# Optimization experiments

Measured on AMD Instinct MI355X. Metric: run time of the kernel, lower is better.

## Reference

```python
import jax, jax.numpy as jnp
import numpy as np

NEG_SLOPE = 0.2  # PyG GATConv default negative_slope


def _gat_layer(x, src, dst, n_nodes, W, a_src, a_dst, b):
    # x: [N, din]; src/dst: [E] (self-loops already included)
    h = x @ W                                  # [N, dout]
    s_src = h @ a_src                          # [N]
    s_dst = h @ a_dst                          # [N]
    e = jax.nn.leaky_relu(s_src[src] + s_dst[dst], NEG_SLOPE)  # [E]
    # per-target-node softmax over incoming edges (stable via segment max)
    m = jax.ops.segment_max(e, dst, num_segments=n_nodes)      # [N]
    a = jnp.exp(e - m[dst])                    # [E]
    denom = jax.ops.segment_sum(a, dst, num_segments=n_nodes)  # [N]
    msg = h[src] * a[:, None]                  # [E, dout]
    agg = jax.ops.segment_sum(msg, dst, num_segments=n_nodes)  # [N, dout]
    return agg / denom[:, None] + b


def setup_inputs() -> dict:
    key = jax.random.key(0)
    ks = jax.random.split(key, 16)
    N, E = 100000, 1600000
    in_dim, hid_dim, out_dim = 128, 128, 64
    x = jax.random.normal(ks[0], (N, in_dim), dtype=jnp.float32)
    edge_idx = jax.random.randint(ks[1], (2, E), 0, N, dtype=jnp.int32)

    def lin(k, din, dout):
        return jax.random.normal(k, (din, dout), dtype=jnp.float32) * (1.0 / np.sqrt(din))

    def att(k, dout):
        return jax.random.normal(k, (dout,), dtype=jnp.float32) * (1.0 / np.sqrt(dout))

    return {
        "x": x, "edge_idx": edge_idx,
        "W1": lin(ks[2], in_dim, hid_dim), "as1": att(ks[3], hid_dim), "ad1": att(ks[4], hid_dim), "b1": jnp.zeros((hid_dim,), jnp.float32),
        "W2": lin(ks[5], hid_dim, hid_dim), "as2": att(ks[6], hid_dim), "ad2": att(ks[7], hid_dim), "b2": jnp.zeros((hid_dim,), jnp.float32),
        "W3": lin(ks[8], hid_dim, out_dim), "as3": att(ks[9], out_dim), "ad3": att(ks[10], out_dim), "b3": jnp.zeros((out_dim,), jnp.float32),
    }


def reference(x, edge_idx, W1, as1, ad1, b1, W2, as2, ad2, b2, W3, as3, ad3, b3):
    N = x.shape[0]
    # add self-loops (PyG GATConv default add_self_loops=True)
    loops = jnp.arange(N, dtype=edge_idx.dtype)
    src = jnp.concatenate([edge_idx[0], loops])
    dst = jnp.concatenate([edge_idx[1], loops])
    h = _gat_layer(x, src, dst, N, W1, as1, ad1, b1)
    h = _gat_layer(h, src, dst, N, W2, as2, ad2, b2)
    h = _gat_layer(h, src, dst, N, W3, as3, ad3, b3)
    return jnp.mean(h, axis=-2)  # [out_dim]
```

## Files before the change

### kernel.cpp

```cpp
#include <hip/hip_runtime.h>

static inline int ceil_div(long long a, long long b) { return (int)((a + b - 1) / b); }

typedef __attribute__((ext_vector_type(8))) short bf16x8;
typedef __attribute__((ext_vector_type(4))) float f32x4;

#define TILE 8192
#define BKSH 9

__device__ __forceinline__ float lrelu(float t) { return t > 0.f ? t : 0.2f * t; }

__device__ __forceinline__ void atomAddF(float* p, float v) {
  unsafeAtomicAdd(p, v);
}

__device__ __forceinline__ unsigned int f2bf(float f) {
  unsigned int u = __float_as_uint(f);
  unsigned int r = ((u >> 16) & 1u) + 0x7fffu;
  return (u + r) >> 16;
}

__global__ void cvt_bf16(const float* __restrict__ X, unsigned short* __restrict__ Xb, int n4) {
  int i = blockIdx.x * blockDim.x + threadIdx.x;
  if (i < n4) {
    const float4 v = ((const float4*)X)[i];
    uint2 o;
    o.x = f2bf(v.x) | (f2bf(v.y) << 16);
    o.y = f2bf(v.z) | (f2bf(v.w) << 16);
    ((uint2*)Xb)[i] = o;
  }
}

__global__ void transpose_all(const float* __restrict__ W1, const float* __restrict__ W2,
                              const float* __restrict__ W3, unsigned short* __restrict__ Wt1,
                              unsigned short* __restrict__ Wt2, unsigned short* __restrict__ Wt3) {
  int idx = blockIdx.x * blockDim.x + threadIdx.x;
  const float* W; unsigned short* Wt; int local, DOUTv;
  if (idx < 16384)      { W = W1; Wt = Wt1; local = idx;          DOUTv = 128; }
  else if (idx < 32768) { W = W2; Wt = Wt2; local = idx - 16384;  DOUTv = 128; }
  else if (idx < 40960) { W = W3; Wt = Wt3; local = idx - 32768;  DOUTv = 64;  }
  else return;
  const int k = local / DOUTv, n = local % DOUTv;
  Wt[n * 128 + k] = (unsigned short)f2bf(W[local]);
}

template<int DOUT>
__launch_bounds__(256)
__global__ void gemm_mfma(const unsigned short* __restrict__ Xb, const unsigned short* __restrict__ Wt,
                          const float* __restrict__ avs, const float* __restrict__ avd,
                          unsigned short* __restrict__ Hb, float* __restrict__ Ss,
                          float* __restrict__ Sd, int N, int RG) {
  constexpr int DIN = 128;
  constexpr int CG = DOUT / 64;
  constexpr int RPB = 4 / CG;
  __shared__ float sps[RPB][2][64], spd[RPB][2][64];

  const int wv = threadIdx.x >> 6;
  const int rgl = wv / CG;
  const int cg  = wv % CG;
  const int rg = blockIdx.x * RPB + rgl;
  const bool active = rg < RG;
  const int lane = threadIdx.x & 63;
  const int l16 = lane & 15, quad = lane >> 4;
  const int row0 = rg * 64, colw0 = cg * 64;

  if (active) {
    int xoff[4], woff[4];
#pragma unroll
    for (int t = 0; t < 4; t++) {
      int m = row0 + t * 16 + l16; if (m > N - 1) m = N - 1;
      xoff[t] = m * DIN + quad * 8;
      woff[t] = (colw0 + t * 16 + l16) * DIN + quad * 8;
    }

    f32x4 acc[4][4];
#pragma unroll
    for (int a = 0; a < 4; a++)
#pragma unroll
      for (int c = 0; c < 4; c++) acc[a][c] = (f32x4)0.f;

#pragma unroll
    for (int kk = 0; kk < 4; kk++) {
      bf16x8 aw[4], bx[4];
#pragma unroll
      for (int t = 0; t < 4; t++) aw[t] = *(const bf16x8*)(Wt + woff[t] + kk * 32);
#pragma unroll
      for (int t = 0; t < 4; t++) bx[t] = *(const bf16x8*)(Xb + xoff[t] + kk * 32);
#pragma unroll
      for (int wt = 0; wt < 4; wt++)
#pragma unroll
        for (int xt = 0; xt < 4; xt++)
          acc[wt][xt] = __builtin_amdgcn_mfma_f32_16x16x32_bf16(aw[wt], bx[xt], acc[wt][xt], 0, 0, 0);
    }

    float4 af[4], df[4];
#pragma unroll
    for (int wt = 0; wt < 4; wt++) {
      af[wt] = *(const float4*)(avs + colw0 + wt * 16 + quad * 4);
      df[wt] = *(const float4*)(avd + colw0 + wt * 16 + quad * 4);
    }
#pragma unroll
    for (int xt = 0; xt < 4; xt++) {
      const int m = row0 + xt * 16 + l16;
      float ps = 0.f, pd = 0.f;
#pragma unroll
      for (int wt = 0; wt < 4; wt++) {
        const f32x4 c = acc[wt][xt];
        ps += c[0]*af[wt].x + c[1]*af[wt].y + c[2]*af[wt].z + c[3]*af[wt].w;
        pd += c[0]*df[wt].x + c[1]*df[wt].y + c[2]*df[wt].z + c[3]*df[wt].w;
      }
      ps += __shfl_xor(ps, 16); ps += __shfl_xor(ps, 32);
      pd += __shfl_xor(pd, 16); pd += __shfl_xor(pd, 32);
      if (quad == 0) {
        if (CG == 2) {
          sps[rgl][cg][xt * 16 + l16] = ps;
          spd[rgl][cg][xt * 16 + l16] = pd;
        } else if (m < N) {
          Ss[m] = ps; Sd[m] = pd;
        }
      }
      if (m < N) {
        unsigned short* hp = Hb + (size_t)m * DOUT + colw0 + quad * 4;
#pragma unroll
        for (int wt = 0; wt < 4; wt++) {
          const f32x4 c = acc[wt][xt];
          uint2 o;
          o.x = f2bf(c[0]) | (f2bf(c[1]) << 16);
          o.y = f2bf(c[2]) | (f2bf(c[3]) << 16);
          *(uint2*)(hp + wt * 16) = o;
        }
      }
    }
  }
  if (CG == 2) {
    __syncthreads();
    if (active && cg == 0) {
      const int m = row0 + lane;
      if (m < N) {
        Ss[m] = sps[rgl][0][lane] + sps[rgl][1][lane];
        Sd[m] = spd[rgl][0][lane] + spd[rgl][1][lane];
      }
    }
  }
}

__launch_bounds__(256)
__global__ void bucket_hist(const int* __restrict__ dstv, int* __restrict__ bh,
                            int E, int NBUK) {
  __shared__ int h[256];
  h[threadIdx.x] = 0;
  __syncthreads();
  const int base = blockIdx.x * TILE;
  const int end = min(E, base + TILE);
  for (int i = base + threadIdx.x; i < end; i += 256)
    atomicAdd(&h[dstv[i] >> BKSH], 1);
  __syncthreads();
  if (threadIdx.x < NBUK) bh[blockIdx.x * NBUK + threadIdx.x] = h[threadIdx.x];
}

__launch_bounds__(256)
__global__ void col_scan(int* __restrict__ bh, int* __restrict__ tot, int NBA, int NBUK) {
  __shared__ int sc[256];
  const int t = threadIdx.x;
  const int b = blockIdx.x;
  int carry = 0;
  for (int c0 = 0; c0 < NBA; c0 += 256) {
    const int idx = c0 + t;
    const int v = (idx < NBA) ? bh[idx * NBUK + b] : 0;
    sc[t] = v;
    __syncthreads();
    for (int off = 1; off < 256; off <<= 1) {
      int u = (t >= off) ? sc[t - off] : 0;
      __syncthreads();
      sc[t] += u;
      __syncthreads();
    }
    if (idx < NBA) bh[idx * NBUK + b] = carry + sc[t] - v;
    carry += sc[255];
    __syncthreads();
  }
  if (t == 0) tot[b] = carry;
}

__launch_bounds__(256)
__global__ void base_scan(const int* __restrict__ tot, int* __restrict__ bucketBase,
                          int* __restrict__ rowptr_N, int NBUK, int E) {
  __shared__ int sc[256];
  const int t = threadIdx.x;
  int carry = 0;
  for (int c0 = 0; c0 < NBUK; c0 += 256) {
    const int idx = c0 + t;
    const int v = (idx < NBUK) ? tot[idx] : 0;
    sc[t] = v;
    __syncthreads();
    for (int off = 1; off < 256; off <<= 1) {
      int u = (t >= off) ? sc[t - off] : 0;
      __syncthreads();
      sc[t] += u;
      __syncthreads();
    }
    if (idx < NBUK) bucketBase[idx] = carry + sc[t] - v;
    carry += sc[255];
    __syncthreads();
  }
  if (t == 0) { bucketBase[NBUK] = E; *rowptr_N = E; }
}

__launch_bounds__(256)
__global__ void bucket_scatter(const int* __restrict__ src, const int* __restrict__ dstv,
                               const int* __restrict__ bh, const int* __restrict__ bucketBase,
                               unsigned int* __restrict__ pairs, int E, int NBUK) {
  __shared__ int ofs[256];
  if (threadIdx.x < NBUK)
    ofs[threadIdx.x] = bh[blockIdx.x * NBUK + threadIdx.x] + bucketBase[threadIdx.x];
  __syncthreads();
  const int base = blockIdx.x * TILE;
  const int end = min(E, base + TILE);
  for (int i = base + threadIdx.x; i < end; i += 256) {
    const int d = dstv[i];
    const int pos = atomicAdd(&ofs[d >> BKSH], 1);
    pairs[pos] = ((unsigned int)src[i] << BKSH) | (unsigned int)(d & ((1 << BKSH) - 1));
  }
}

__launch_bounds__(256)
__global__ void region_build(const unsigned int* __restrict__ pairs,
                             const int* __restrict__ bucketBase,
                             int* __restrict__ rowptr, int* __restrict__ srcs, int N) {
  __shared__ int cnt[512], ofs[512], ps[256];
  const int t = threadIdx.x;
  const int r = blockIdx.x;
  const int p0 = bucketBase[r], p1 = bucketBase[r + 1];
  cnt[t] = 0; cnt[t + 256] = 0;
  __syncthreads();
  for (int i = p0 + t; i < p1; i += 256)
    atomicAdd(&cnt[pairs[i] & 511u], 1);
  __syncthreads();
  const int c0 = cnt[2 * t], c1 = cnt[2 * t + 1];
  const int pr = c0 + c1;
  ps[t] = pr;
  __syncthreads();
  for (int off = 1; off < 256; off <<= 1) {
    int v = (t >= off) ? ps[t - off] : 0;
    __syncthreads();
    ps[t] += v;
    __syncthreads();
  }
  const int pbase = ps[t] - pr;
  ofs[2 * t] = pbase; ofs[2 * t + 1] = pbase + c0;
  __syncthreads();
  {
    const int d0 = (r << BKSH) + t;
    if (d0 < N) rowptr[d0] = p0 + ofs[t];
    const int d1 = (r << BKSH) + t + 256;
    if (d1 < N) rowptr[d1] = p0 + ofs[t + 256];
  }
  __syncthreads();
  for (int i = p0 + t; i < p1; i += 256) {
    const unsigned int w = pairs[i];
    const int pos = atomicAdd(&ofs[w & 511u], 1);
    srcs[p0 + pos] = (int)(w >> BKSH);
  }
}

template<int DOUT, bool OBF>
__launch_bounds__(256)
__global__ void node_gather(const int* __restrict__ rowptr, const int* __restrict__ srcs,
                            const float* __restrict__ Ss, const float* __restrict__ Sd,
                            const unsigned short* __restrict__ Hb, const float* __restrict__ b,
                            float* __restrict__ out, unsigned short* __restrict__ outb, int N) {
  constexpr int EPL = DOUT / 16;
  __shared__ uint2 swL[16][18];

  const int l16 = threadIdx.x & 15;
  const int grp = threadIdx.x >> 4;
  const int node = blockIdx.x * 16 + grp;
  if (node >= N) return;

  const int r0 = rowptr[node], r1 = rowptr[node + 1];
  const int deg = r1 - r0;
  const float sd = Sd[node];
  const float wself = __expf(lrelu(Ss[node] + sd));

  float acc[EPL];
#pragma unroll
  for (int k = 0; k < EPL; k++) acc[k] = 0.f;
  float lsum = 0.f;
  const size_t colb = (size_t)l16 * EPL;

  for (int j0 = 0; j0 < deg; j0 += 16) {
    const int idx = j0 + l16;
    int s = node; float w = 0.f;
    if (idx < deg) {
      s = srcs[r0 + idx];
      w = __expf(lrelu(Ss[s] + sd));
    }
    lsum += w;
    swL[grp][l16] = make_uint2((unsigned)s, __float_as_uint(w));
    const int cnt = min(16, deg - j0);
    int t = 0;
    for (; t + 4 <= cnt; t += 4) {
      const uint2 sw0 = swL[grp][t],     sw1 = swL[grp][t + 1];
      const uint2 sw2 = swL[grp][t + 2], sw3 = swL[grp][t + 3];
      const float w0 = __uint_as_float(sw0.y), w1 = __uint_as_float(sw1.y);
      const float w2 = __uint_as_float(sw2.y), w3 = __uint_as_float(sw3.y);
      if (EPL == 8) {
        const uint4 u0 = *(const uint4*)(Hb + (size_t)sw0.x * DOUT + colb);
        const uint4 u1 = *(const uint4*)(Hb + (size_t)sw1.x * DOUT + colb);
        const uint4 u2 = *(const uint4*)(Hb + (size_t)sw2.x * DOUT + colb);
        const uint4 u3 = *(const uint4*)(Hb + (size_t)sw3.x * DOUT + colb);
        const unsigned int a0[4] = {u0.x,u0.y,u0.z,u0.w}, a1[4] = {u1.x,u1.y,u1.z,u1.w};
        const unsigned int a2[4] = {u2.x,u2.y,u2.z,u2.w}, a3[4] = {u3.x,u3.y,u3.z,u3.w};
#pragma unroll
        for (int k = 0; k < 4; k++) {
          acc[2*k]   += __uint_as_float(a0[k] << 16) * w0 + __uint_as_float(a1[k] << 16) * w1
                      + __uint_as_float(a2[k] << 16) * w2 + __uint_as_float(a3[k] << 16) * w3;
          acc[2*k+1] += __uint_as_float(a0[k] & 0xffff0000u) * w0 + __uint_as_float(a1[k] & 0xffff0000u) * w1
                      + __uint_as_float(a2[k] & 0xffff0000u) * w2 + __uint_as_float(a3[k] & 0xffff0000u) * w3;
        }
      } else {
        const uint2 u0 = *(const uint2*)(Hb + (size_t)sw0.x * DOUT + colb);
        const uint2 u1 = *(const uint2*)(Hb + (size_t)sw1.x * DOUT + colb);
        const uint2 u2 = *(const uint2*)(Hb + (size_t)sw2.x * DOUT + colb);
        const uint2 u3 = *(const uint2*)(Hb + (size_t)sw3.x * DOUT + colb);
        const unsigned int a0[2] = {u0.x,u0.y}, a1[2] = {u1.x,u1.y};
        const unsigned int a2[2] = {u2.x,u2.y}, a3[2] = {u3.x,u3.y};
#pragma unroll
        for (int k = 0; k < 2; k++) {
          acc[2*k]   += __uint_as_float(a0[k] << 16) * w0 + __uint_as_float(a1[k] << 16) * w1
                      + __uint_as_float(a2[k] << 16) * w2 + __uint_as_float(a3[k] << 16) * w3;
          acc[2*k+1] += __uint_as_float(a0[k] & 0xffff0000u) * w0 + __uint_as_float(a1[k] & 0xffff0000u) * w1
                      + __uint_as_float(a2[k] & 0xffff0000u) * w2 + __uint_as_float(a3[k] & 0xffff0000u) * w3;
        }
      }
    }
    for (; t < cnt; t++) {
      const uint2 sw = swL[grp][t];
      const float w0 = __uint_as_float(sw.y);
      const unsigned short* pp = Hb + (size_t)sw.x * DOUT + colb;
#pragma unroll
      for (int k = 0; k < EPL / 2; k++) {
        const unsigned int u = ((const unsigned int*)pp)[k];
        acc[2*k]   += __uint_as_float(u << 16) * w0;
        acc[2*k+1] += __uint_as_float(u & 0xffff0000u) * w0;
      }
    }
  }

#pragma unroll
  for (int off = 8; off; off >>= 1) lsum += __shfl_xor(lsum, off);

  {
    const unsigned short* pp = Hb + (size_t)node * DOUT + colb;
#pragma unroll
    for (int k = 0; k < EPL / 2; k++) {
      const unsigned int u = ((const unsigned int*)pp)[k];
      acc[2*k]   += __uint_as_float(u << 16) * wself;
      acc[2*k+1] += __uint_as_float(u & 0xffff0000u) * wself;
    }
  }
  const float inv = 1.f / (lsum + wself);

  float o[EPL];
#pragma unroll
  for (int k = 0; k < EPL; k++) o[k] = acc[k] * inv + b[colb + k];
  if (OBF) {
    if (EPL == 8) {
      uint4 u;
      u.x = f2bf(o[0]) | (f2bf(o[1]) << 16);
      u.y = f2bf(o[2]) | (f2bf(o[3]) << 16);
      u.z = f2bf(o[4]) | (f2bf(o[5]) << 16);
      u.w = f2bf(o[6]) | (f2bf(o[7]) << 16);
      *(uint4*)(outb + (size_t)node * DOUT + colb) = u;
    } else {
      uint2 u;
      u.x = f2bf(o[0]) | (f2bf(o[1]) << 16);
      u.y = f2bf(o[2]) | (f2bf(o[3]) << 16);
      *(uint2*)(outb + (size_t)node * DOUT + colb) = u;
    }
  } else {
    float* op = out + (size_t)node * DOUT + colb;
#pragma unroll
    for (int k = 0; k < EPL; k += 4)
      *(float4*)(op + k) = make_float4(o[k], o[k+1], o[k+2], o[k+3]);
  }
}

__global__ void mean64(const float* __restrict__ Hf, float* __restrict__ out, int N, float scale) {
  __shared__ float sm[256];
  const int col = threadIdx.x & 63;
  const int seg = threadIdx.x >> 6;
  const int stride = gridDim.x * 4;
  float s = 0.f;
  for (int n = blockIdx.x * 4 + seg; n < N; n += stride) s += Hf[(size_t)n * 64 + col];
  sm[threadIdx.x] = s;
  __syncthreads();
  if (seg == 0) {
    float tot = sm[col] + sm[64 + col] + sm[128 + col] + sm[192 + col];
    atomAddF(&out[col], tot * scale);
  }
}

extern "C" void kernel_launch(void* const* d_in, const int* in_sizes, int n_in,
                              void* d_out, int out_size, void* d_ws, size_t ws_size,
                              hipStream_t stream) {
  const float* x   = (const float*)d_in[0];
  const int*   ei  = (const int*)d_in[1];
  const float* W1  = (const float*)d_in[2];
  const float* as1 = (const float*)d_in[3];
  const float* ad1 = (const float*)d_in[4];
  const float* b1  = (const float*)d_in[5];
  const float* W2  = (const float*)d_in[6];
  const float* as2 = (const float*)d_in[7];
  const float* ad2 = (const float*)d_in[8];
  const float* b2  = (const float*)d_in[9];
  const float* W3  = (const float*)d_in[10];
  const float* as3 = (const float*)d_in[11];
  const float* ad3 = (const float*)d_in[12];
  const float* b3  = (const float*)d_in[13];

  const int N = in_sizes[0] / 128;
  const int E = in_sizes[1] / 2;
  const int* src  = ei;
  const int* dstv = ei + E;
  const int RG = ceil_div(N, 64);
  const int NBA = ceil_div(E, TILE);
  const int NBUK = ceil_div(N, 1 << BKSH);

  float* p = (float*)d_ws;
  float* bufA = p; p += (size_t)N * 64;
  float* SsSd = p; p += (size_t)2 * N;
  float* Ss = SsSd, *Sd = SsSd + N;
  unsigned short* Xb = (unsigned short*)p; p += (size_t)N * 64;
  unsigned short* Hb = (unsigned short*)p; p += (size_t)N * 64;
  unsigned short* Wt1 = (unsigned short*)p; p += 128 * 128 / 2;
  unsigned short* Wt2 = (unsigned short*)p; p += 128 * 128 / 2;
  unsigned short* Wt3 = (unsigned short*)p; p += 128 * 64 / 2;
  int* ip = (int*)p;
  int* rowptr     = ip; ip += N + 1;
  int* bh         = ip; ip += (size_t)NBA * NBUK;
  int* tot        = ip; ip += NBUK;
  int* bucketBase = ip; ip += NBUK + 1;
  unsigned int* pairs = (unsigned int*)ip; ip += E;
  int* srcs       = ip; ip += E;

  bucket_hist<<<NBA, 256, 0, stream>>>(dstv, bh, E, NBUK);
  col_scan<<<NBUK, 256, 0, stream>>>(bh, tot, NBA, NBUK);
  base_scan<<<1, 256, 0, stream>>>(tot, bucketBase, rowptr + N, NBUK, E);
  bucket_scatter<<<NBA, 256, 0, stream>>>(src, dstv, bh, bucketBase, pairs, E, NBUK);
  region_build<<<NBUK, 256, 0, stream>>>(pairs, bucketBase, rowptr, srcs, N);

  transpose_all<<<ceil_div(40960, 256), 256, 0, stream>>>(W1, W2, W3, Wt1, Wt2, Wt3);
  cvt_bf16<<<ceil_div((long long)N * 32, 256), 256, 0, stream>>>(x, Xb, N * 32);

  const int GG = ceil_div(N, 16);
  gemm_mfma<128><<<ceil_div(RG, 2), 256, 0, stream>>>(Xb, Wt1, as1, ad1, Hb, Ss, Sd, N, RG);
  node_gather<128, true><<<GG, 256, 0, stream>>>(rowptr, srcs, Ss, Sd, Hb, b1, nullptr, Xb, N);
  gemm_mfma<128><<<ceil_div(RG, 2), 256, 0, stream>>>(Xb, Wt2, as2, ad2, Hb, Ss, Sd, N, RG);
  node_gather<128, true><<<GG, 256, 0, stream>>>(rowptr, srcs, Ss, Sd, Hb, b2, nullptr, Xb, N);
  gemm_mfma<64><<<ceil_div(RG, 4), 256, 0, stream>>>(Xb, Wt3, as3, ad3, Hb, Ss, Sd, N, RG);
  node_gather<64, false><<<GG, 256, 0, stream>>>(rowptr, srcs, Ss, Sd, Hb, b3, bufA, nullptr, N);

  hipMemsetAsync(d_out, 0, 64 * sizeof(float), stream);
  mean64<<<256, 256, 0, stream>>>(bufA, (float*)d_out, N, 1.0f / (float)N);
}
```

Before: 432.1 us.

## Stage block-wide edge weights cooperatively and fuse final-layer mean into gather

The gather kernel now has all 256 threads of a block compute source indices and attention weights for the block's 16 nodes' edges together. The results go into a 512-entry shared window, and a small binary search over the block's row pointers finds each edge's destination. This replaces per-node 16-edge chunks and is meant to balance the uneven degree distribution and cut per-group serialization. The inner loop now issues 8 feature loads at once, and tail edges are padded in groups of 4. For the last layer, per-block column sums go to a small partial buffer instead of a full N×64 output, and the mean kernel reduces only those partials.

After: 432.4 us. No clear change (+0.1%).

```diff
diff --git a/kernel.cpp b/kernel.cpp
--- a/kernel.cpp
+++ b/kernel.cpp
@@ -263,86 +263,133 @@
   }
 }
 
-template<int DOUT, bool OBF>
+template<int DOUT, bool OBF, bool MEANRED>
 __launch_bounds__(256)
 __global__ void node_gather(const int* __restrict__ rowptr, const int* __restrict__ srcs,
                             const float* __restrict__ Ss, const float* __restrict__ Sd,
                             const unsigned short* __restrict__ Hb, const float* __restrict__ b,
                             float* __restrict__ out, unsigned short* __restrict__ outb, int N) {
   constexpr int EPL = DOUT / 16;
-  __shared__ uint2 swL[16][18];
-
-  const int l16 = threadIdx.x & 15;
-  const int grp = threadIdx.x >> 4;
-  const int node = blockIdx.x * 16 + grp;
-  if (node >= N) return;
-
-  const int r0 = rowptr[node], r1 = rowptr[node + 1];
-  const int deg = r1 - r0;
-  const float sd = Sd[node];
-  const float wself = __expf(lrelu(Ss[node] + sd));
+  constexpr int WIN = 512;
+  __shared__ uint2 s_sw[WIN];
+  __shared__ int   rp[17];
+  __shared__ float sdv[16];
+  __shared__ float s_mean[64];
+
+  const int tid = threadIdx.x;
+  const int l16 = tid & 15;
+  const int grp = tid >> 4;
+  const int node0 = blockIdx.x * 16;
+  const int node = node0 + grp;
+  const bool nvalid = node < N;
+
+  if (tid < 17) rp[tid] = rowptr[min(node0 + tid, N)];
+  if (tid < 16) sdv[tid] = (node0 + tid < N) ? Sd[node0 + tid] : 0.f;
+  if (MEANRED && tid < 64) s_mean[tid] = 0.f;
+  __syncthreads();
+
+  const int base = rp[0], endE = rp[16];
+  const int r0 = rp[grp], r1 = rp[grp + 1];
+  const float sd = sdv[grp];
 
   float acc[EPL];
 #pragma unroll
   for (int k = 0; k < EPL; k++) acc[k] = 0.f;
   float lsum = 0.f;
-  const size_t colb = (size_t)l16 * EPL;
-
-  for (int j0 = 0; j0 < deg; j0 += 16) {
-    const int idx = j0 + l16;
-    int s = node; float w = 0.f;
-    if (idx < deg) {
-      s = srcs[r0 + idx];
-      w = __expf(lrelu(Ss[s] + sd));
-    }
-    lsum += w;
-    swL[grp][l16] = make_uint2((unsigned)s, __float_as_uint(w));
-    const int cnt = min(16, deg - j0);
+  const int colb = l16 * EPL;
+
+  for (int wb = base; wb < endE; wb += WIN) {
+    if (wb != base) __syncthreads();
+#pragma unroll
+    for (int k0 = 0; k0 < WIN; k0 += 256) {
+      const int k = k0 + tid;
+      const int i = wb + k;
+      if (i < endE) {
+        const int s = srcs[i];
+        int o = 0;
+#pragma unroll
+        for (int st = 8; st; st >>= 1)
+          if (rp[o + st] <= i) o += st;
+        const float w = __expf(lrelu(Ss[s] + sdv[o]));
+        s_sw[k] = make_uint2((unsigned)s, __float_as_uint(w));
+      }
+    }
+    __syncthreads();
+
+    const int lo = max(r0, wb), hi = min(r1, wb + WIN);
+    const int cnt = hi - lo;
+    const int L = lo - wb;
+    for (int t = l16; t < cnt; t += 16) lsum += __uint_as_float(s_sw[L + t].y);
+
     int t = 0;
-    for (; t + 4 <= cnt; t += 4) {
-      const uint2 sw0 = swL[grp][t],     sw1 = swL[grp][t + 1];
-      const uint2 sw2 = swL[grp][t + 2], sw3 = swL[grp][t + 3];
-      const float w0 = __uint_as_float(sw0.y), w1 = __uint_as_float(sw1.y);
-      const float w2 = __uint_as_float(sw2.y), w3 = __uint_as_float(sw3.y);
+    for (; t + 8 <= cnt; t += 8) {
+      uint2 sw[8];
+#pragma unroll
+      for (int q = 0; q < 8; q++) sw[q] = s_sw[L + t + q];
       if (EPL == 8) {
-        const uint4 u0 = *(const uint4*)(Hb + (size_t)sw0.x * DOUT + colb);
-        const uint4 u1 = *(const uint4*)(Hb + (size_t)sw1.x * DOUT + colb);
-        const uint4 u2 = *(const uint4*)(Hb + (size_t)sw2.x * DOUT + colb);
-        const uint4 u3 = *(const uint4*)(Hb + (size_t)sw3.x * DOUT + colb);
-        const unsigned int a0[4] = {u0.x,u0.y,u0.z,u0.w}, a1[4] = {u1.x,u1.y,u1.z,u1.w};
-        const unsigned int a2[4] = {u2.x,u2.y,u2.z,u2.w}, a3[4] = {u3.x,u3.y,u3.z,u3.w};
-#pragma unroll
-        for (int k = 0; k < 4; k++) {
-          acc[2*k]   += __uint_as_float(a0[k] << 16) * w0 + __uint_as_float(a1[k] << 16) * w1
-                      + __uint_as_float(a2[k] << 16) * w2 + __uint_as_float(a3[k] << 16) * w3;
-          acc[2*k+1] += __uint_as_float(a0[k] & 0xffff0000u) * w0 + __uint_as_float(a1[k] & 0xffff0000u) * w1
-                      + __uint_as_float(a2[k] & 0xffff0000u) * w2 + __uint_as_float(a3[k] & 0xffff0000u) * w3;
+        uint4 u[8];
+#pragma unroll
+        for (int q = 0; q < 8; q++) u[q] = *(const uint4*)(Hb + ((size_t)sw[q].x * DOUT) + colb);
+#pragma unroll
+        for (int q = 0; q < 8; q++) {
+          const float w = __uint_as_float(sw[q].y);
+          const unsigned int a[4] = {u[q].x, u[q].y, u[q].z, u[q].w};
+#pragma unroll
+          for (int k = 0; k < 4; k++) {
+            acc[2*k]   += __uint_as_float(a[k] << 16) * w;
+            acc[2*k+1] += __uint_as_float(a[k] & 0xffff0000u) * w;
+          }
         }
       } else {
-        const uint2 u0 = *(const uint2*)(Hb + (size_t)sw0.x * DOUT + colb);
-        const uint2 u1 = *(const uint2*)(Hb + (size_t)sw1.x * DOUT + colb);
-        const uint2 u2 = *(const uint2*)(Hb + (size_t)sw2.x * DOUT + colb);
-        const uint2 u3 = *(const uint2*)(Hb + (size_t)sw3.x * DOUT + colb);
-        const unsigned int a0[2] = {u0.x,u0.y}, a1[2] = {u1.x,u1.y};
-        const unsigned int a2[2] = {u2.x,u2.y}, a3[2] = {u3.x,u3.y};
-#pragma unroll
-        for (int k = 0; k < 2; k++) {
-          acc[2*k]   += __uint_as_float(a0[k] << 16) * w0 + __uint_as_float(a1[k] << 16) * w1
-                      + __uint_as_float(a2[k] << 16) * w2 + __uint_as_float(a3[k] << 16) * w3;
-          acc[2*k+1] += __uint_as_float(a0[k] & 0xffff0000u) * w0 + __uint_as_float(a1[k] & 0xffff0000u) * w1
-                      + __uint_as_float(a2[k] & 0xffff0000u) * w2 + __uint_as_float(a3[k] & 0xffff0000u) * w3;
+        uint2 u[8];
+#pragma unroll
+        for (int q = 0; q < 8; q++) u[q] = *(const uint2*)(Hb + ((size_t)sw[q].x * DOUT) + colb);
+#pragma unroll
+        for (int q = 0; q < 8; q++) {
+          const float w = __uint_as_float(sw[q].y);
+          const unsigned int a[2] = {u[q].x, u[q].y};
+#pragma unroll
+          for (int k = 0; k < 2; k++) {
+            acc[2*k]   += __uint_as_float(a[k] << 16) * w;
+            acc[2*k+1] += __uint_as_float(a[k] & 0xffff0000u) * w;
+          }
         }
       }
     }
-    for (; t < cnt; t++) {
-      const uint2 sw = swL[grp][t];
-      const float w0 = __uint_as_float(sw.y);
-      const unsigned short* pp = Hb + (size_t)sw.x * DOUT + colb;
-#pragma unroll
-      for (int k = 0; k < EPL / 2; k++) {
-        const unsigned int u = ((const unsigned int*)pp)[k];
-        acc[2*k]   += __uint_as_float(u << 16) * w0;
-        acc[2*k+1] += __uint_as_float(u & 0xffff0000u) * w0;
+    for (; t < cnt; t += 4) {
+      uint2 sw[4]; float wv[4];
+#pragma unroll
+      for (int q = 0; q < 4; q++) {
+        const int tt = min(t + q, cnt - 1);
+        sw[q] = s_sw[L + tt];
+        wv[q] = (t + q < cnt) ? __uint_as_float(sw[q].y) : 0.f;
+      }
+      if (EPL == 8) {
+        uint4 u[4];
+#pragma unroll
+        for (int q = 0; q < 4; q++) u[q] = *(const uint4*)(Hb + ((size_t)sw[q].x * DOUT) + colb);
+#pragma unroll
+        for (int q = 0; q < 4; q++) {
+          const unsigned int a[4] = {u[q].x, u[q].y, u[q].z, u[q].w};
+#pragma unroll
+          for (int k = 0; k < 4; k++) {
+            acc[2*k]   += __uint_as_float(a[k] << 16) * wv[q];
+            acc[2*k+1] += __uint_as_float(a[k] & 0xffff0000u) * wv[q];
+          }
+        }
+      } else {
+        uint2 u[4];
+#pragma unroll
+        for (int q = 0; q < 4; q++) u[q] = *(const uint2*)(Hb + ((size_t)sw[q].x * DOUT) + colb);
+#pragma unroll
+        for (int q = 0; q < 4; q++) {
+          const unsigned int a[2] = {u[q].x, u[q].y};
+#pragma unroll
+          for (int k = 0; k < 2; k++) {
+            acc[2*k]   += __uint_as_float(a[k] << 16) * wv[q];
+            acc[2*k+1] += __uint_as_float(a[k] & 0xffff0000u) * wv[q];
+          }
+        }
       }
     }
   }
@@ -350,7 +397,9 @@
 #pragma unroll
   for (int off = 8; off; off >>= 1) lsum += __shfl_xor(lsum, off);
 
-  {
+  float wself = 0.f;
+  if (nvalid) {
+    wself = __expf(lrelu(Ss[node] + sd));
     const unsigned short* pp = Hb + (size_t)node * DOUT + colb;
 #pragma unroll
     for (int k = 0; k < EPL / 2; k++) {
@@ -359,30 +408,39 @@
       acc[2*k+1] += __uint_as_float(u & 0xffff0000u) * wself;
     }
   }
-  const float inv = 1.f / (lsum + wself);
-
-  float o[EPL];
-#pragma unroll
-  for (int k = 0; k < EPL; k++) o[k] = acc[k] * inv + b[colb + k];
-  if (OBF) {
-    if (EPL == 8) {
-      uint4 u;
-      u.x = f2bf(o[0]) | (f2bf(o[1]) << 16);
-      u.y = f2bf(o[2]) | (f2bf(o[3]) << 16);
-      u.z = f2bf(o[4]) | (f2bf(o[5]) << 16);
-      u.w = f2bf(o[6]) | (f2bf(o[7]) << 16);
-      *(uint4*)(outb + (size_t)node * DOUT + colb) = u;
+
+  if (nvalid) {
+    const float inv = 1.f / (lsum + wself);
+    float o[EPL];
+#pragma unroll
+    for (int k = 0; k < EPL; k++) o[k] = acc[k] * inv + b[colb + k];
+    if (MEANRED) {
+#pragma unroll
+      for (int k = 0; k < EPL; k++) atomicAdd(&s_mean[colb + k], o[k]);
+    } else if (OBF) {
+      if (EPL == 8) {
+        uint4 u;
+        u.x = f2bf(o[0]) | (f2bf(o[1]) << 16);
+        u.y = f2bf(o[2]) | (f2bf(o[3]) << 16);
+        u.z = f2bf(o[4]) | (f2bf(o[5]) << 16);
+        u.w = f2bf(o[6]) | (f2bf(o[7]) << 16);
+        *(uint4*)(outb + (size_t)node * DOUT + colb) = u;
+      } else {
+        uint2 u;
+        u.x = f2bf(o[0]) | (f2bf(o[1]) << 16);
+        u.y = f2bf(o[2]) | (f2bf(o[3]) << 16);
+        *(uint2*)(outb + (size_t)node * DOUT + colb) = u;
+      }
     } else {
-      uint2 u;
-      u.x = f2bf(o[0]) | (f2bf(o[1]) << 16);
-      u.y = f2bf(o[2]) | (f2bf(o[3]) << 16);
-      *(uint2*)(outb + (size_t)node * DOUT + colb) = u;
-    }
-  } else {
-    float* op = out + (size_t)node * DOUT + colb;
-#pragma unroll
-    for (int k = 0; k < EPL; k += 4)
-      *(float4*)(op + k) = make_float4(o[k], o[k+1], o[k+2], o[k+3]);
+      float* op = out + (size_t)node * DOUT + colb;
+#pragma unroll
+      for (int k = 0; k < EPL; k += 4)
+        *(float4*)(op + k) = make_float4(o[k], o[k+1], o[k+2], o[k+3]);
+    }
+  }
+  if (MEANRED) {
+    __syncthreads();
+    if (tid < 64) out[(size_t)blockIdx.x * 64 + tid] = s_mean[tid];
   }
 }
 
@@ -426,9 +484,10 @@
   const int RG = ceil_div(N, 64);
   const int NBA = ceil_div(E, TILE);
   const int NBUK = ceil_div(N, 1 << BKSH);
+  const int GG = ceil_div(N, 16);
 
   float* p = (float*)d_ws;
-  float* bufA = p; p += (size_t)N * 64;
+  float* part = p; p += (size_t)GG * 64;
   float* SsSd = p; p += (size_t)2 * N;
   float* Ss = SsSd, *Sd = SsSd + N;
   unsigned short* Xb = (unsigned short*)p; p += (size_t)N * 64;
@@ -453,14 +512,13 @@
   transpose_all<<<ceil_div(40960, 256), 256, 0, stream>>>(W1, W2, W3, Wt1, Wt2, Wt3);
   cvt_bf16<<<ceil_div((long long)N * 32, 256), 256, 0, stream>>>(x, Xb, N * 32);
 
-  const int GG = ceil_div(N, 16);
   gemm_mfma<128><<<ceil_div(RG, 2), 256, 0, stream>>>(Xb, Wt1, as1, ad1, Hb, Ss, Sd, N, RG);
-  node_gather<128, true><<<GG, 256, 0, stream>>>(rowptr, srcs, Ss, Sd, Hb, b1, nullptr, Xb, N);
+  node_gather<128, true, false><<<GG, 256, 0, stream>>>(rowptr, srcs, Ss, Sd, Hb, b1, nullptr, Xb, N);
   gemm_mfma<128><<<ceil_div(RG, 2), 256, 0, stream>>>(Xb, Wt2, as2, ad2, Hb, Ss, Sd, N, RG);
-  node_gather<128, true><<<GG, 256, 0, stream>>>(rowptr, srcs, Ss, Sd, Hb, b2, nullptr, Xb, N);
+  node_gather<128, true, false><<<GG, 256, 0, stream>>>(rowptr, srcs, Ss, Sd, Hb, b2, nullptr, Xb, N);
   gemm_mfma<64><<<ceil_div(RG, 4), 256, 0, stream>>>(Xb, Wt3, as3, ad3, Hb, Ss, Sd, N, RG);
-  node_gather<64, false><<<GG, 256, 0, stream>>>(rowptr, srcs, Ss, Sd, Hb, b3, bufA, nullptr, N);
+  node_gather<64, false, true><<<GG, 256, 0, stream>>>(rowptr, srcs, Ss, Sd, Hb, b3, part, nullptr, N);
 
   hipMemsetAsync(d_out, 0, 64 * sizeof(float), stream);
-  mean64<<<256, 256, 0, stream>>>(bufA, (float*)d_out, N, 1.0f / (float)N);
-}
+  mean64<<<256, 256, 0, stream>>>(part, (float*)d_out, GG, 1.0f / (float)N);
+}
```
